# Kernel tuning notes

Measured on AMD Instinct MI355X. Metric: run time of the kernel, lower is better.

Reference implementation:

```python
import jax, jax.numpy as jnp
import numpy as np

# Static layer configuration (from init_kwargs)
C_IN, H, W = 8, 32, 32
C_OUT, KH, KW = 16, 3, 3
SH, SW = 1, 1
PH, PW = 1, 1
OH = (H + 2 * PH - KH) // SH + 1
OW = (W + 2 * PW - KW) // SW + 1
N_IN = C_IN * H * W      # 8192 input-layer neurons
N_OUT = C_OUT * OH * OW  # 16384 output-layer neurons


def setup_inputs() -> dict:
    key = jax.random.key(0)
    k1, k2, k3, k4 = jax.random.split(key, 4)
    base = jax.random.normal(k1, (C_IN, H, W), dtype=jnp.float32)
    rad = jax.random.uniform(k2, (C_IN, H, W), dtype=jnp.float32)
    return {
        "concrete_lower": base - rad,   # ensure lower <= upper
        "concrete_upper": base + rad,
        "weights": jax.random.normal(k3, (C_OUT, C_IN, KH, KW), dtype=jnp.float32) * 0.1,
        "bias": jax.random.normal(k4, (C_OUT,), dtype=jnp.float32) * 0.1,
    }


def build_abstract_matrix(weights, bias):
    """Vectorized equivalent of _create_conv2d_channel_v0 over all channels.

    Produces M of shape (N_IN+1, N_OUT+1): column (c*OH*OW + i*OW + j) holds the
    affine coefficients (over flattened input neurons, bias in last row) of
    output pixel (c, i, j); last column is the homogeneous [0...0, 1] column.
    """
    idy = jnp.arange(OH)[:, None] * SH - PH + jnp.arange(KH)[None, :]  # (OH, KH)
    idx = jnp.arange(OW)[:, None] * SW - PW + jnp.arange(KW)[None, :]  # (OW, KW)
    valid = (((idy >= 0) & (idy < H))[:, :, None, None]
             & ((idx >= 0) & (idx < W))[None, None, :, :])             # (OH, KH, OW, KW)

    cin = jnp.arange(C_IN)
    # broadcast layout: (C_OUT, C_IN, OH, KH, OW, KW)
    rows = (cin[None, :, None, None, None, None] * (H * W)
            + idy[None, None, :, :, None, None] * W
            + idx[None, None, None, None, :, :])
    oc = jnp.arange(C_OUT)
    cols = (oc[:, None, None, None, None, None] * (OH * OW)
            + jnp.arange(OH)[None, None, :, None, None, None] * OW
            + jnp.arange(OW)[None, None, None, None, :, None])
    vals = weights[:, :, None, :, None, :]  # (C_OUT, C_IN, 1, KH, 1, KW)

    shape = (C_OUT, C_IN, OH, KH, OW, KW)
    rows_b = jnp.broadcast_to(rows, shape).reshape(-1)
    cols_b = jnp.broadcast_to(cols, shape).reshape(-1)
    vals_b = jnp.broadcast_to(vals, shape).reshape(-1)
    valid_b = jnp.broadcast_to(valid[None, None], shape).reshape(-1)
    # padding taps (out of input bounds) -> out-of-range row index, dropped by scatter
    rows_b = jnp.where(valid_b, rows_b, N_IN + 1)

    M = jnp.zeros((N_IN + 1, N_OUT + 1), dtype=jnp.float32)
    M = M.at[rows_b, cols_b].set(vals_b, mode="drop")
    M = M.at[N_IN, :N_OUT].set(jnp.repeat(bias, OH * OW))  # bias row per output pixel
    M = M.at[N_IN, N_OUT].set(1.0)                          # homogeneous corner
    return M


def back_substitute(M, l_in, u_in, lower=True):
    # Interval evaluation of the affine map: positive coeffs pair with one bound,
    # negative with the other; last row of M is the bias.
    Wc = M[:-1, :]
    b = M[-1, :]
    pos = jnp.maximum(Wc, 0.0)
    neg = jnp.minimum(Wc, 0.0)
    if lower:
        return l_in @ pos + u_in @ neg + b
    return u_in @ pos + l_in @ neg + b


def reference(concrete_lower, concrete_upper, weights, bias):
    M = build_abstract_matrix(weights, bias)  # abstract lower == upper for a conv layer
    l = concrete_lower.reshape(-1)
    u = concrete_upper.reshape(-1)
    lo = back_substitute(M, l, u, lower=True)[:N_OUT].reshape(C_OUT, OH, OW)
    hi = back_substitute(M, l, u, lower=False)[:N_OUT].reshape(C_OUT, OH, OW)
    return (lo, hi, M)
```

## Files before the change

kernel.cpp:

```cpp
#include <hip/hip_runtime.h>

#define C_IN  8
#define H     32
#define W     32
#define C_OUT 16
#define KH    3
#define KW    3
#define OH    32
#define OW    32
#define N_IN  (C_IN * H * W)
#define N_OUT (C_OUT * OH * OW)
#define MROWS (N_IN + 1)
#define MCOLS (N_OUT + 1)

#define ROWS_PER_BLOCK 4
#define N_ROW_BLOCKS   (N_IN / ROWS_PER_BLOCK)
#define N_BOUND_BLOCKS 64

typedef float v4f __attribute__((ext_vector_type(4)));

__global__ __launch_bounds__(256) void fused_kernel(const float* __restrict__ l_in,
                                                    const float* __restrict__ u_in,
                                                    const float* __restrict__ wts,
                                                    const float* __restrict__ bias,
                                                    float* __restrict__ out,
                                                    float* __restrict__ M) {
    const int b = blockIdx.x;
    const int t = threadIdx.x;

    if (b < N_BOUND_BLOCKS) {
        int tid = b * 256 + t;
        int c = tid >> 10;
        int i = (tid >> 5) & 31;
        int j = tid & 31;

        float lo = bias[c];
        float hi = lo;

        #pragma unroll
        for (int cin = 0; cin < C_IN; ++cin) {
            #pragma unroll
            for (int kh = 0; kh < KH; ++kh) {
                int iy = i - 1 + kh;
                if ((unsigned)iy >= (unsigned)H) continue;
                #pragma unroll
                for (int kw = 0; kw < KW; ++kw) {
                    int ix = j - 1 + kw;
                    if ((unsigned)ix >= (unsigned)W) continue;
                    float w = wts[c * 72 + cin * 9 + kh * 3 + kw];
                    int   r = cin * 1024 + iy * 32 + ix;
                    float a  = w * l_in[r];
                    float bb = w * u_in[r];
                    lo += fminf(a, bb);
                    hi += fmaxf(a, bb);
                }
            }
        }
        out[tid]         = lo;
        out[N_OUT + tid] = hi;
        return;
    }

    if (b == N_BOUND_BLOCKS) {
        float* __restrict__ Mrow = M + (size_t)N_IN * MCOLS;
        #pragma unroll
        for (int k = 0; k < 16; ++k) {
            float bv = bias[k];
            v4f v = {bv, bv, bv, bv};
            __builtin_nontemporal_store(v, (v4f*)(Mrow + (k << 10) + 4 * t));
        }
        if (t == 0) Mrow[N_OUT] = 1.0f;
        return;
    }

    const int g   = b - (N_BOUND_BLOCKS + 1);
    const int r0  = g * ROWS_PER_BLOCK;
    const int cin = r0 >> 10;

    __shared__ float ldsW[160];
    if (t < 144) {
        int c = t / 9, r = t - 9 * c;
        ldsW[t] = wts[c * 72 + cin * 9 + r];
    } else if (t < 160) {
        ldsW[t] = 0.0f;
    }
    __syncthreads();

    for (int rr = 0; rr < ROWS_PER_BLOCK; ++rr) {
        const int row = r0 + rr;
        const int iy  = (row >> 5) & 31;
        const int ix  = row & 31;

        float* __restrict__ Mrow = M + (size_t)row * MCOLS;
        const int p    = (4 - (row & 3)) & 3;
        const int Nf   = (MCOLS - p) >> 2;
        const int tail = MCOLS - p - 4 * Nf;

        if (t < p) {
            int kh = iy + 1, kw = ix + 1 - t;
            bool ok = ((unsigned)kh < 3u) & ((unsigned)kw < 3u);
            Mrow[t] = ok ? ldsW[kh * 3 + kw] : 0.0f;
        }
        if (t < tail) {
            int col = p + 4 * Nf + t;
            float v = 0.0f;
            if (col < N_OUT) {
                int c = col >> 10, i = (col >> 5) & 31, j = col & 31;
                int kh = iy + 1 - i, kw = ix + 1 - j;
                if (((unsigned)kh < 3u) & ((unsigned)kw < 3u)) v = ldsW[c * 9 + kh * 3 + kw];
            }
            Mrow[col] = v;
        }

        int  add9[4];
        bool okq[4];
        int  klim[4];
        const int e0 = p + 4 * t;
        #pragma unroll
        for (int q = 0; q < 4; ++q) {
            int e     = e0 + q;
            int carry = e >> 10;
            int em    = e & 1023;
            int i = em >> 5, j = em & 31;
            int kh = iy + 1 - i, kw = ix + 1 - j;
            bool ok = ((unsigned)kh < 3u) & ((unsigned)kw < 3u);
            okq[q]  = ok;
            add9[q] = carry * 9 + (ok ? kh * 3 + kw : 0);
            klim[q] = 16 - carry;
        }

        float* dst = Mrow + p + 4 * t;
        #pragma unroll
        for (int k = 0; k < 16; ++k) {
            int idx = (k << 8) + t;
            if (idx < Nf) {
                float vv[4];
                #pragma unroll
                for (int q = 0; q < 4; ++q) {
                    float w = ldsW[k * 9 + add9[q]];
                    vv[q] = (okq[q] & (k < klim[q])) ? w : 0.0f;
                }
                v4f v4 = {vv[0], vv[1], vv[2], vv[3]};
                __builtin_nontemporal_store(v4, (v4f*)(dst + (k << 10)));
            }
        }
    }
}

extern "C" void kernel_launch(void* const* d_in, const int* in_sizes, int n_in,
                              void* d_out, int out_size, void* d_ws, size_t ws_size,
                              hipStream_t stream) {
    const float* lower = (const float*)d_in[0];
    const float* upper = (const float*)d_in[1];
    const float* wts   = (const float*)d_in[2];
    const float* bias  = (const float*)d_in[3];

    float* out = (float*)d_out;
    float* M   = out + 2 * N_OUT;

    const int grid = N_BOUND_BLOCKS + 1 + N_ROW_BLOCKS;
    hipLaunchKernelGGL(fused_kernel, dim3(grid), dim3(256), 0, stream,
                       lower, upper, wts, bias, out, M);
}
```

Before: 558.1 us.

## Flatten M fill into grid-stride float4 stream over whole matrix

Replaces the per-row fill, where each block handled four rows with peel and tail logic, with a flat loop. A fixed grid of 2048 blocks walks the first N_IN rows of M as contiguous aligned float4s, tracking row and column incrementally and handling row wraps inside each vector. The whole weight tensor is staged in LDS, and launch bounds request higher occupancy. The aim is fully coalesced, uniformly sized streaming writes without per-row edge handling, at the cost of more index arithmetic per vector.

```diff
diff --git a/kernel.cpp b/kernel.cpp
--- a/kernel.cpp
+++ b/kernel.cpp
@@ -13,18 +13,22 @@
 #define MROWS (N_IN + 1)
 #define MCOLS (N_OUT + 1)
 
-#define ROWS_PER_BLOCK 4
-#define N_ROW_BLOCKS   (N_IN / ROWS_PER_BLOCK)
 #define N_BOUND_BLOCKS 64
+#define N_FLAT_BLOCKS  2048
+#define ITER_F4     (N_FLAT_BLOCKS * 256)
+#define N_FULL_ITER 64
+#define TAIL_BLKS   8
+#define STEP_ROW 127
+#define STEP_COL 16257
 
 typedef float v4f __attribute__((ext_vector_type(4)));
 
-__global__ __launch_bounds__(256) void fused_kernel(const float* __restrict__ l_in,
-                                                    const float* __restrict__ u_in,
-                                                    const float* __restrict__ wts,
-                                                    const float* __restrict__ bias,
-                                                    float* __restrict__ out,
-                                                    float* __restrict__ M) {
+__global__ __launch_bounds__(256, 8) void fused_kernel(const float* __restrict__ l_in,
+                                                       const float* __restrict__ u_in,
+                                                       const float* __restrict__ wts,
+                                                       const float* __restrict__ bias,
+                                                       float* __restrict__ out,
+                                                       float* __restrict__ M) {
     const int b = blockIdx.x;
     const int t = threadIdx.x;
 
@@ -73,77 +77,50 @@
         return;
     }
 
-    const int g   = b - (N_BOUND_BLOCKS + 1);
-    const int r0  = g * ROWS_PER_BLOCK;
-    const int cin = r0 >> 10;
+    const int fb = b - (N_BOUND_BLOCKS + 1);
 
-    __shared__ float ldsW[160];
-    if (t < 144) {
-        int c = t / 9, r = t - 9 * c;
-        ldsW[t] = wts[c * 72 + cin * 9 + r];
-    } else if (t < 160) {
-        ldsW[t] = 0.0f;
-    }
+    __shared__ float ldsW[C_OUT * C_IN * 9];
+    for (int s = t; s < C_OUT * C_IN * 9; s += 256) ldsW[s] = wts[s];
     __syncthreads();
 
-    for (int rr = 0; rr < ROWS_PER_BLOCK; ++rr) {
-        const int row = r0 + rr;
-        const int iy  = (row >> 5) & 31;
-        const int ix  = row & 31;
+    const int f0 = fb * 256 + t;
+    const int e0 = f0 * 4;
+    int row = e0 >> 14;
+    int col = (e0 & 16383) - row;
+    if (col < 0) { col += MCOLS; row -= 1; }
 
-        float* __restrict__ Mrow = M + (size_t)row * MCOLS;
-        const int p    = (4 - (row & 3)) & 3;
-        const int Nf   = (MCOLS - p) >> 2;
-        const int tail = MCOLS - p - 4 * Nf;
+    float* dst = M + (size_t)e0;
 
-        if (t < p) {
-            int kh = iy + 1, kw = ix + 1 - t;
-            bool ok = ((unsigned)kh < 3u) & ((unsigned)kw < 3u);
-            Mrow[t] = ok ? ldsW[kh * 3 + kw] : 0.0f;
-        }
-        if (t < tail) {
-            int col = p + 4 * Nf + t;
-            float v = 0.0f;
-            if (col < N_OUT) {
-                int c = col >> 10, i = (col >> 5) & 31, j = col & 31;
-                int kh = iy + 1 - i, kw = ix + 1 - j;
-                if (((unsigned)kh < 3u) & ((unsigned)kw < 3u)) v = ldsW[c * 9 + kh * 3 + kw];
-            }
-            Mrow[col] = v;
-        }
+    for (int n = 0; n < N_FULL_ITER + 1; ++n) {
+        if (n == N_FULL_ITER && fb >= TAIL_BLKS) break;
 
-        int  add9[4];
-        bool okq[4];
-        int  klim[4];
-        const int e0 = p + 4 * t;
+        float vv[4];
         #pragma unroll
         for (int q = 0; q < 4; ++q) {
-            int e     = e0 + q;
-            int carry = e >> 10;
-            int em    = e & 1023;
-            int i = em >> 5, j = em & 31;
-            int kh = iy + 1 - i, kw = ix + 1 - j;
-            bool ok = ((unsigned)kh < 3u) & ((unsigned)kw < 3u);
-            okq[q]  = ok;
-            add9[q] = carry * 9 + (ok ? kh * 3 + kw : 0);
-            klim[q] = 16 - carry;
+            int  cq    = col + q;
+            bool carry = (cq >= MCOLS);
+            int  cq2   = carry ? cq - MCOLS : cq;
+            int  rq    = row + (carry ? 1 : 0);
+            int  cin   = rq >> 10;
+            int  iy    = (rq >> 5) & 31;
+            int  ix    = rq & 31;
+            int  c     = cq2 >> 10;
+            int  i     = (cq2 >> 5) & 31;
+            int  j     = cq2 & 31;
+            int  kh    = iy + 1 - i;
+            int  kw    = ix + 1 - j;
+            bool ok    = ((unsigned)kh < 3u) & ((unsigned)kw < 3u) & (cq2 < N_OUT);
+            int  idx   = ok ? (c * 72 + cin * 9 + kh * 3 + kw) : 0;
+            float w    = ldsW[idx];
+            vv[q]      = ok ? w : 0.0f;
         }
+        v4f v4 = {vv[0], vv[1], vv[2], vv[3]};
+        __builtin_nontemporal_store(v4, (v4f*)dst);
 
-        float* dst = Mrow + p + 4 * t;
-        #pragma unroll
-        for (int k = 0; k < 16; ++k) {
-            int idx = (k << 8) + t;
-            if (idx < Nf) {
-                float vv[4];
-                #pragma unroll
-                for (int q = 0; q < 4; ++q) {
-                    float w = ldsW[k * 9 + add9[q]];
-                    vv[q] = (okq[q] & (k < klim[q])) ? w : 0.0f;
-                }
-                v4f v4 = {vv[0], vv[1], vv[2], vv[3]};
-                __builtin_nontemporal_store(v4, (v4f*)(dst + (k << 10)));
-            }
-        }
+        dst += (size_t)4 * ITER_F4;
+        row += STEP_ROW;
+        col += STEP_COL;
+        if (col >= MCOLS) { col -= MCOLS; row += 1; }
     }
 }
 
@@ -158,7 +135,7 @@
     float* out = (float*)d_out;
     float* M   = out + 2 * N_OUT;
 
-    const int grid = N_BOUND_BLOCKS + 1 + N_ROW_BLOCKS;
+    const int grid = N_BOUND_BLOCKS + 1 + N_FLAT_BLOCKS;
     hipLaunchKernelGGL(fused_kernel, dim3(grid), dim3(256), 0, stream,
                        lower, upper, wts, bias, out, M);
 }
```

Result: faster. 546.9 us (-2.0%).
